# Kernel optimization log

Measured on AMD Instinct MI355X. Metric: run time of the kernel, lower is better.

Reference implementation:

```python
import jax, jax.numpy as jnp
import numpy as np

# Fixed problem sizes (uniform frames so the irregular loop vectorizes)
S = 32            # number of frames (sequences)
N = 128           # pedestrians per frame
H = 64            # pool_h_dim (lstm hidden dim)
G = 8             # grid_size
NS = 2.0          # neighbourhood_size
OUT = 64          # pool_out_dim
EPS = 1e-5        # BatchNorm1d eps


def setup_inputs() -> dict:
    key = jax.random.key(0)
    k1, k2, k3 = jax.random.split(key, 3)
    hidden_states = jax.random.normal(k1, (S * N, H), jnp.float32)
    # positions in [0, 4): neighbourhood of size 2 captures many neighbours
    all_pos = jax.random.uniform(k2, (S * N, 2), jnp.float32) * 4.0
    W = jax.random.normal(k3, (G * G * H, OUT), jnp.float32) * 0.02
    b = jnp.zeros((OUT,), jnp.float32)
    gamma = jnp.ones((OUT,), jnp.float32)
    beta = jnp.zeros((OUT,), jnp.float32)
    starts = jnp.arange(S, dtype=jnp.int32) * N
    seq_start_end = jnp.stack([starts, starts + N], axis=1)
    return {"hidden_states": hidden_states, "all_pos": all_pos, "W": W,
            "b": b, "gamma": gamma, "beta": beta,
            "seq_start_end": seq_start_end}


def _pool_one_frame(hs, ps):
    # hs: [N, H] hidden states, ps: [N, 2] positions of one frame.
    # Pair (i, j): bbox around ped i, contribution from ped j's hidden state.
    xi, yi = ps[:, 0][:, None], ps[:, 1][:, None]   # bbox owner i -> rows
    xj, yj = ps[:, 0][None, :], ps[:, 1][None, :]   # neighbour j -> cols
    half = NS / 2
    tlx, tly = xi - half, yi + half                 # top-left of bbox(i)
    brx, bry = xi + half, yi - half                 # bottom-right of bbox(i)
    gx = jnp.floor((xj - tlx) / NS * G)
    gy = jnp.floor((tly - yj) / NS * G)
    grid = (gx + G * gy).astype(jnp.int32) + 1      # +1: slot 0 is dump bin
    # out-of-bbox or self -> masked to bin 0
    mask = ((xj <= tlx) | (yj >= tly) | (xj >= brx) | (yj <= bry)
            | jnp.eye(N, dtype=bool))
    grid = grid + (jnp.arange(N, dtype=jnp.int32) * (G * G))[:, None]
    grid = jnp.where(mask, 0, grid)                 # [N, N]
    vals = jnp.broadcast_to(hs[None, :, :], (N, N, H)).reshape(N * N, H)
    pooled = jax.ops.segment_sum(vals, grid.reshape(-1),
                                 num_segments=N * G * G + 1)[1:]
    return pooled.reshape(N, G * G * H)


def reference(hidden_states, all_pos, W, b, gamma, beta, seq_start_end):
    h = hidden_states.reshape(S, N, H)
    p = all_pos.reshape(S, N, 2)
    pool_h = jax.vmap(_pool_one_frame)(h, p).reshape(S * N, G * G * H)
    x = pool_h @ W + b
    # BatchNorm1d in training mode: biased batch statistics
    mean = jnp.mean(x, axis=0)
    var = jnp.mean((x - mean) ** 2, axis=0)
    x = (x - mean) / jnp.sqrt(var + EPS) * gamma + beta
    return jax.nn.relu(x)
```

## Files before the change

### kernel.cpp

```cpp
#include <hip/hip_runtime.h>
#include <math.h>

#define NFRAMES 32
#define NPED    128
#define HDIM    64
#define KDIM    4096
#define OUTD    64
#define EPSV    1e-5f
#define NBLK    256
#define MROW    16
#define PROW    4104
#define HROWW   68

typedef __attribute__((ext_vector_type(8))) short  short8;
typedef __attribute__((ext_vector_type(4))) float  floatx4;

static __device__ __forceinline__ unsigned short f2bf(float f) {
    union { float f; unsigned u; } v; v.f = f;
    unsigned r = v.u + 0x7fffu + ((v.u >> 16) & 1u);
    return (unsigned short)(r >> 16);
}
static __device__ __forceinline__ unsigned pk2bf(float a, float b) {
    return (unsigned)f2bf(a) | ((unsigned)f2bf(b) << 16);
}

static __device__ __forceinline__ int kperm(int k) {
    return (k & 0xC0F) | ((k >> 2) & 0x0F0) | ((k & 0x030) << 4);
}

__global__ void k_wt(const float* __restrict__ W, unsigned short* __restrict__ Wt) {
    __shared__ float T[64 * 65];
    const int t  = threadIdx.x;
    const int k0 = blockIdx.x * 64;
    #pragma unroll
    for (int it = 0; it < 8; ++it) {
        int idx = it * 512 + t;
        int kl = idx >> 6, o = idx & 63;
        T[kl * 65 + o] = W[(size_t)(k0 + kl) * OUTD + o];
    }
    __syncthreads();
    {
        int o  = t & 63;
        int kl = (t >> 6) * 8;
        unsigned pk[4];
        #pragma unroll
        for (int e = 0; e < 4; ++e)
            pk[e] = pk2bf(T[(kl + 2 * e) * 65 + o], T[(kl + 2 * e + 1) * 65 + o]);
        int klog = kperm(k0 + kl);
        int wn   = o >> 4;
        int q    = klog >> 10;
        int s    = (klog >> 5) & 31;
        int quad = (klog >> 3) & 3;
        int ln   = quad * 16 + (o & 15);
        unsigned short* dst = Wt + ((size_t)((wn * 4 + q) * 32 + s) * 64 + ln) * 8;
        *(uint4*)dst = (uint4){pk[0], pk[1], pk[2], pk[3]};
    }
}

__global__ __launch_bounds__(1024, 1) void k_fused(
    const float* __restrict__ hs, const float* __restrict__ pos,
    const unsigned short* __restrict__ Wt,
    float* __restrict__ x, float* __restrict__ psumT, float* __restrict__ psumsqT)
{
    __shared__ char SM[MROW * PROW * 2 + 2048];
    unsigned short* P    = (unsigned short*)SM;
    unsigned int*   HsTw = (unsigned int*)SM;
    float*          red  = (float*)SM;
    unsigned char*  CT   = (unsigned char*)(SM + MROW * PROW * 2);

    const int tid   = threadIdx.x;
    const int bid   = blockIdx.x;
    const int f     = bid >> 3;
    const int chunk = bid & 7;
    const int lane  = tid & 63;
    const int w     = tid >> 6;
    const int m     = lane & 15;
    const int quad  = lane >> 4;

    const float4* h4 = (const float4*)(hs + f * (NPED * HDIM));
    {
        int jp   = (tid & 31) + ((tid >> 9) << 5);
        int hidx = (tid >> 5) & 15;
        float4 va = h4[(2 * jp) * 16 + hidx];
        float4 vb = h4[(2 * jp + 1) * 16 + hidx];
        HsTw[(hidx * 4 + 0) * HROWW + jp] = pk2bf(va.x, vb.x);
        HsTw[(hidx * 4 + 1) * HROWW + jp] = pk2bf(va.y, vb.y);
        HsTw[(hidx * 4 + 2) * HROWW + jp] = pk2bf(va.z, vb.z);
        HsTw[(hidx * 4 + 3) * HROWW + jp] = pk2bf(va.w, vb.w);
    }
    const float2* pf = (const float2*)pos + f * NPED;
    const int i0 = chunk * 16;
    #pragma unroll
    for (int it = 0; it < 2; ++it) {
        int idx = it * 1024 + tid;
        int i = idx >> 7, j = idx & 127;
        float2 pi = pf[i0 + i];
        float2 pj = pf[j];
        float tlx = pi.x - 1.0f, tly = pi.y + 1.0f;
        bool valid = (pj.x > tlx) & (pj.y < tly) & (pj.x < pi.x + 1.0f) &
                     (pj.y > pi.y - 1.0f) & (j != i0 + i);
        int gx = (int)floorf((pj.x - tlx) * 4.0f);
        int gy = (int)floorf((tly - pj.y) * 4.0f);
        int c  = gx + 8 * gy;
        CT[i * NPED + j] = (valid && (unsigned)c < 64u) ? (unsigned char)c : 255;
    }
    __syncthreads();

    short8 Af[4][4];
    #pragma unroll
    for (int ht = 0; ht < 4; ++ht)
        #pragma unroll
        for (int kt = 0; kt < 4; ++kt)
            Af[ht][kt] = *(const short8*)&HsTw[(ht * 16 + m) * HROWW + kt * 16 + quad * 4];
    __syncthreads();

    {
        const int i = w;
        const unsigned char* ctRow = CT + i * NPED;
        #pragma unroll
        for (int ch = 0; ch < 2; ++ch) {
            floatx4 pa[4][2];
            #pragma unroll
            for (int ht = 0; ht < 4; ++ht)
                #pragma unroll
                for (int c2 = 0; c2 < 2; ++c2) pa[ht][c2] = (floatx4){0.f, 0.f, 0.f, 0.f};
            #pragma unroll
            for (int kt = 0; kt < 4; ++kt) {
                unsigned long long cb = *(const unsigned long long*)(ctRow + kt * 32 + quad * 8);
                unsigned lo = (unsigned)cb, hi = (unsigned)(cb >> 32);
                int b0 = (int)(lo & 255u), b1 = (int)((lo >> 8) & 255u);
                int b2 = (int)((lo >> 16) & 255u), b3 = (int)(lo >> 24);
                int b4 = (int)(hi & 255u), b5 = (int)((hi >> 8) & 255u);
                int b6 = (int)((hi >> 16) & 255u), b7 = (int)(hi >> 24);
                #pragma unroll
                for (int c2 = 0; c2 < 2; ++c2) {
                    const int tgt = (ch * 2 + c2) * 16 + m;
                    union { int iv[4]; short8 sv; } B;
                    B.iv[0] = (b0 == tgt ? 0x00003F80 : 0) | (b1 == tgt ? 0x3F800000 : 0);
                    B.iv[1] = (b2 == tgt ? 0x00003F80 : 0) | (b3 == tgt ? 0x3F800000 : 0);
                    B.iv[2] = (b4 == tgt ? 0x00003F80 : 0) | (b5 == tgt ? 0x3F800000 : 0);
                    B.iv[3] = (b6 == tgt ? 0x00003F80 : 0) | (b7 == tgt ? 0x3F800000 : 0);
                    #pragma unroll
                    for (int ht = 0; ht < 4; ++ht)
                        pa[ht][c2] = __builtin_amdgcn_mfma_f32_16x16x32_bf16(Af[ht][kt], B.sv, pa[ht][c2], 0, 0, 0);
                }
            }
            #pragma unroll
            for (int c2 = 0; c2 < 2; ++c2)
                #pragma unroll
                for (int ht = 0; ht < 4; ++ht) {
                    union { floatx4 fv; unsigned uv[4]; } U; U.fv = pa[ht][c2];
                    uint2 pv;
                    pv.x = __builtin_amdgcn_perm(U.uv[1], U.uv[0], 0x07060302u);
                    pv.y = __builtin_amdgcn_perm(U.uv[3], U.uv[2], 0x07060302u);
                    *reinterpret_cast<uint2*>(&P[i * PROW + (ch * 2 + c2) * 1024 + ht * 256 + m * 16 + quad * 4]) = pv;
                }
        }
    }
    __syncthreads();

    const int wn = w & 3;
    const int wq = w >> 2;
    floatx4 acc[4];
    #pragma unroll
    for (int u = 0; u < 4; ++u) acc[u] = (floatx4){0.f, 0.f, 0.f, 0.f};
    const unsigned short* Prow = P + m * PROW + wq * 1024;
    const unsigned short* wB   = Wt + ((size_t)(wn * 4 + wq) * 32 * 64 + lane) * 8;
    #pragma unroll 8
    for (int s = 0; s < 32; ++s) {
        short8 a = *(const short8*)(Prow + s * 32 + quad * 8);
        short8 b = *(const short8*)(wB + s * 512);
        acc[s & 3] = __builtin_amdgcn_mfma_f32_16x16x32_bf16(a, b, acc[s & 3], 0, 0, 0);
    }
    floatx4 accf = (acc[0] + acc[1]) + (acc[2] + acc[3]);
    __syncthreads();

    if (wq != 0) *(floatx4*)(red + (((wq - 1) * 4 + wn) * 64 + lane) * 4) = accf;
    __syncthreads();

    if (wq == 0) {
        accf += *(const floatx4*)(red + ((0 * 4 + wn) * 64 + lane) * 4);
        accf += *(const floatx4*)(red + ((1 * 4 + wn) * 64 + lane) * 4);
        accf += *(const floatx4*)(red + ((2 * 4 + wn) * 64 + lane) * 4);
        const int ibase = f * NPED + chunk * 16;
        float s1 = 0.f, s2 = 0.f;
        #pragma unroll
        for (int r = 0; r < 4; ++r) {
            float v = accf[r];
            int row = quad * 4 + r;
            x[(size_t)(ibase + row) * OUTD + wn * 16 + m] = v;
            s1 += v; s2 += v * v;
        }
        s1 += __shfl_xor(s1, 16); s1 += __shfl_xor(s1, 32);
        s2 += __shfl_xor(s2, 16); s2 += __shfl_xor(s2, 32);
        if (lane < 16) {
            psumT  [(wn * 16 + lane) * NBLK + bid] = s1;
            psumsqT[(wn * 16 + lane) * NBLK + bid] = s2;
        }
    }
}

__global__ __launch_bounds__(512) void k_apply(
    const float* __restrict__ x, const float* __restrict__ psumT,
    const float* __restrict__ psumsqT, const float* __restrict__ gamma,
    const float* __restrict__ beta, float* __restrict__ out) {
    __shared__ float muL[OUTD], isL[OUTD];
    const int t = threadIdx.x;
    const int o = t >> 3, p = t & 7;
    float s1 = 0.f, s2 = 0.f;
    const float4* q1 = (const float4*)(psumT   + o * NBLK + p * 32);
    const float4* q2 = (const float4*)(psumsqT + o * NBLK + p * 32);
    #pragma unroll
    for (int i = 0; i < 8; ++i) {
        float4 a = q1[i], b = q2[i];
        s1 += (a.x + a.y) + (a.z + a.w);
        s2 += (b.x + b.y) + (b.z + b.w);
    }
    #pragma unroll
    for (int d = 1; d < 8; d <<= 1) {
        s1 += __shfl_xor(s1, d);
        s2 += __shfl_xor(s2, d);
    }
    if (p == 0) {
        const float inv_n = 1.0f / (float)(NFRAMES * NPED);
        float mu  = s1 * inv_n;
        float var = s2 * inv_n - mu * mu;
        muL[o] = mu;
        isL[o] = rsqrtf(var + EPSV);
    }
    __syncthreads();
    #pragma unroll
    for (int i = 0; i < 4; ++i) {
        int g  = blockIdx.x * 2048 + i * 512 + t;
        int o0 = (g & 15) * 4;
        float4 xv = ((const float4*)x)[g];
        float4 r;
        r.x = (xv.x - muL[o0 + 0]) * isL[o0 + 0] * gamma[o0 + 0] + beta[o0 + 0];
        r.y = (xv.y - muL[o0 + 1]) * isL[o0 + 1] * gamma[o0 + 1] + beta[o0 + 1];
        r.z = (xv.z - muL[o0 + 2]) * isL[o0 + 2] * gamma[o0 + 2] + beta[o0 + 2];
        r.w = (xv.w - muL[o0 + 3]) * isL[o0 + 3] * gamma[o0 + 3] + beta[o0 + 3];
        r.x = r.x > 0.f ? r.x : 0.f;
        r.y = r.y > 0.f ? r.y : 0.f;
        r.z = r.z > 0.f ? r.z : 0.f;
        r.w = r.w > 0.f ? r.w : 0.f;
        ((float4*)out)[g] = r;
    }
}

extern "C" void kernel_launch(void* const* d_in, const int* in_sizes, int n_in,
                              void* d_out, int out_size, void* d_ws, size_t ws_size,
                              hipStream_t stream) {
    const float* hs    = (const float*)d_in[0];
    const float* pos   = (const float*)d_in[1];
    const float* W     = (const float*)d_in[2];
    const float* gamma = (const float*)d_in[4];
    const float* beta  = (const float*)d_in[5];

    char* ws = (char*)d_ws;
    unsigned short* Wt = (unsigned short*)ws;
    float* x       = (float*)(ws + (512 << 10));
    float* psumT   = (float*)(ws + (512 << 10) + (1 << 20));
    float* psumsqT = psumT + NBLK * OUTD;

    k_wt   <<<KDIM / 64, 512, 0, stream>>>(W, Wt);
    k_fused<<<NBLK, 1024, 0, stream>>>(hs, pos, Wt, x, psumT, psumsqT);
    k_apply<<<32, 512, 0, stream>>>(x, psumT, psumsqT, gamma, beta, (float*)d_out);
}
```

Before: 87.05 us.

## Merge weight transpose, pooling GEMM and batchnorm into one cooperative kernel

Replaces the three launches (weight transpose/convert, fused pool+GEMM, batchnorm apply) with a single cooperative kernel. Each block converts a 16-row slice of W to bf16 in the permuted layout, then a grid-wide sync separates that from the GEMM. A second grid sync follows the per-block partial sums, after which every block reduces the batch statistics itself and applies normalization and ReLU directly from its accumulators. This removes two launch gaps and the round trip of the intermediate x through global memory. In exchange it adds two grid barriers and redundant statistics reduction in all 256 blocks, and it requires all 256 blocks of 1024 threads to be co-resident.

```diff
diff --git a/kernel.cpp b/kernel.cpp
--- a/kernel.cpp
+++ b/kernel.cpp
@@ -1,5 +1,8 @@
 #include <hip/hip_runtime.h>
+#include <hip/hip_cooperative_groups.h>
 #include <math.h>
+
+namespace cg = cooperative_groups;
 
 #define NFRAMES 32
 #define NPED    128
@@ -28,44 +31,20 @@
     return (k & 0xC0F) | ((k >> 2) & 0x0F0) | ((k & 0x030) << 4);
 }
 
-__global__ void k_wt(const float* __restrict__ W, unsigned short* __restrict__ Wt) {
-    __shared__ float T[64 * 65];
-    const int t  = threadIdx.x;
-    const int k0 = blockIdx.x * 64;
-    #pragma unroll
-    for (int it = 0; it < 8; ++it) {
-        int idx = it * 512 + t;
-        int kl = idx >> 6, o = idx & 63;
-        T[kl * 65 + o] = W[(size_t)(k0 + kl) * OUTD + o];
-    }
-    __syncthreads();
-    {
-        int o  = t & 63;
-        int kl = (t >> 6) * 8;
-        unsigned pk[4];
-        #pragma unroll
-        for (int e = 0; e < 4; ++e)
-            pk[e] = pk2bf(T[(kl + 2 * e) * 65 + o], T[(kl + 2 * e + 1) * 65 + o]);
-        int klog = kperm(k0 + kl);
-        int wn   = o >> 4;
-        int q    = klog >> 10;
-        int s    = (klog >> 5) & 31;
-        int quad = (klog >> 3) & 3;
-        int ln   = quad * 16 + (o & 15);
-        unsigned short* dst = Wt + ((size_t)((wn * 4 + q) * 32 + s) * 64 + ln) * 8;
-        *(uint4*)dst = (uint4){pk[0], pk[1], pk[2], pk[3]};
-    }
-}
-
-__global__ __launch_bounds__(1024, 1) void k_fused(
+__global__ __launch_bounds__(1024, 1) void k_all(
     const float* __restrict__ hs, const float* __restrict__ pos,
-    const unsigned short* __restrict__ Wt,
-    float* __restrict__ x, float* __restrict__ psumT, float* __restrict__ psumsqT)
+    const float* __restrict__ W, const float* __restrict__ gamma,
+    const float* __restrict__ beta, unsigned short* __restrict__ Wt,
+    float* __restrict__ psumT, float* __restrict__ psumsqT,
+    float* __restrict__ out)
 {
     __shared__ char SM[MROW * PROW * 2 + 2048];
     unsigned short* P    = (unsigned short*)SM;
     unsigned int*   HsTw = (unsigned int*)SM;
     float*          red  = (float*)SM;
+    float*          muL  = (float*)(SM + 16384);
+    float*          isL  = (float*)(SM + 16640);
+    float*          Tw   = (float*)(SM + 24576);
     unsigned char*  CT   = (unsigned char*)(SM + MROW * PROW * 2);
 
     const int tid   = threadIdx.x;
@@ -76,7 +55,13 @@
     const int w     = tid >> 6;
     const int m     = lane & 15;
     const int quad  = lane >> 4;
-
+    const int wn    = w & 3;
+    const int wq    = w >> 2;
+
+    {
+        int kl = tid >> 6, o = tid & 63;
+        Tw[kl * 65 + o] = W[(size_t)(bid * 16 + kl) * OUTD + o];
+    }
     const float4* h4 = (const float4*)(hs + f * (NPED * HDIM));
     {
         int jp   = (tid & 31) + ((tid >> 9) << 5);
@@ -106,6 +91,22 @@
     }
     __syncthreads();
 
+    if (tid < 128) {
+        int o  = tid & 63;
+        int kl = (tid >> 6) * 8;
+        unsigned pk[4];
+        #pragma unroll
+        for (int e = 0; e < 4; ++e)
+            pk[e] = pk2bf(Tw[(kl + 2 * e) * 65 + o], Tw[(kl + 2 * e + 1) * 65 + o]);
+        int klog = kperm(bid * 16 + kl);
+        int on   = o >> 4;
+        int q    = klog >> 10;
+        int s    = (klog >> 5) & 31;
+        int qd   = (klog >> 3) & 3;
+        int ln   = qd * 16 + (o & 15);
+        unsigned short* dst = Wt + ((size_t)((on * 4 + q) * 32 + s) * 64 + ln) * 8;
+        *(uint4*)dst = (uint4){pk[0], pk[1], pk[2], pk[3]};
+    }
     short8 Af[4][4];
     #pragma unroll
     for (int ht = 0; ht < 4; ++ht)
@@ -115,8 +116,7 @@
     __syncthreads();
 
     {
-        const int i = w;
-        const unsigned char* ctRow = CT + i * NPED;
+        const unsigned char* ctRow = CT + w * NPED;
         #pragma unroll
         for (int ch = 0; ch < 2; ++ch) {
             floatx4 pa[4][2];
@@ -153,14 +153,14 @@
                     uint2 pv;
                     pv.x = __builtin_amdgcn_perm(U.uv[1], U.uv[0], 0x07060302u);
                     pv.y = __builtin_amdgcn_perm(U.uv[3], U.uv[2], 0x07060302u);
-                    *reinterpret_cast<uint2*>(&P[i * PROW + (ch * 2 + c2) * 1024 + ht * 256 + m * 16 + quad * 4]) = pv;
+                    *reinterpret_cast<uint2*>(&P[w * PROW + (ch * 2 + c2) * 1024 + ht * 256 + m * 16 + quad * 4]) = pv;
                 }
         }
     }
     __syncthreads();
 
-    const int wn = w & 3;
-    const int wq = w >> 2;
+    cg::this_grid().sync();
+
     floatx4 acc[4];
     #pragma unroll
     for (int u = 0; u < 4; ++u) acc[u] = (floatx4){0.f, 0.f, 0.f, 0.f};
@@ -182,15 +182,9 @@
         accf += *(const floatx4*)(red + ((0 * 4 + wn) * 64 + lane) * 4);
         accf += *(const floatx4*)(red + ((1 * 4 + wn) * 64 + lane) * 4);
         accf += *(const floatx4*)(red + ((2 * 4 + wn) * 64 + lane) * 4);
-        const int ibase = f * NPED + chunk * 16;
         float s1 = 0.f, s2 = 0.f;
         #pragma unroll
-        for (int r = 0; r < 4; ++r) {
-            float v = accf[r];
-            int row = quad * 4 + r;
-            x[(size_t)(ibase + row) * OUTD + wn * 16 + m] = v;
-            s1 += v; s2 += v * v;
-        }
+        for (int r = 0; r < 4; ++r) { s1 += accf[r]; s2 += accf[r] * accf[r]; }
         s1 += __shfl_xor(s1, 16); s1 += __shfl_xor(s1, 32);
         s2 += __shfl_xor(s2, 16); s2 += __shfl_xor(s2, 32);
         if (lane < 16) {
@@ -198,52 +192,47 @@
             psumsqT[(wn * 16 + lane) * NBLK + bid] = s2;
         }
     }
-}
-
-__global__ __launch_bounds__(512) void k_apply(
-    const float* __restrict__ x, const float* __restrict__ psumT,
-    const float* __restrict__ psumsqT, const float* __restrict__ gamma,
-    const float* __restrict__ beta, float* __restrict__ out) {
-    __shared__ float muL[OUTD], isL[OUTD];
-    const int t = threadIdx.x;
-    const int o = t >> 3, p = t & 7;
-    float s1 = 0.f, s2 = 0.f;
-    const float4* q1 = (const float4*)(psumT   + o * NBLK + p * 32);
-    const float4* q2 = (const float4*)(psumsqT + o * NBLK + p * 32);
-    #pragma unroll
-    for (int i = 0; i < 8; ++i) {
-        float4 a = q1[i], b = q2[i];
-        s1 += (a.x + a.y) + (a.z + a.w);
-        s2 += (b.x + b.y) + (b.z + b.w);
-    }
-    #pragma unroll
-    for (int d = 1; d < 8; d <<= 1) {
-        s1 += __shfl_xor(s1, d);
-        s2 += __shfl_xor(s2, d);
-    }
-    if (p == 0) {
-        const float inv_n = 1.0f / (float)(NFRAMES * NPED);
-        float mu  = s1 * inv_n;
-        float var = s2 * inv_n - mu * mu;
-        muL[o] = mu;
-        isL[o] = rsqrtf(var + EPSV);
-    }
-    __syncthreads();
-    #pragma unroll
-    for (int i = 0; i < 4; ++i) {
-        int g  = blockIdx.x * 2048 + i * 512 + t;
-        int o0 = (g & 15) * 4;
-        float4 xv = ((const float4*)x)[g];
-        float4 r;
-        r.x = (xv.x - muL[o0 + 0]) * isL[o0 + 0] * gamma[o0 + 0] + beta[o0 + 0];
-        r.y = (xv.y - muL[o0 + 1]) * isL[o0 + 1] * gamma[o0 + 1] + beta[o0 + 1];
-        r.z = (xv.z - muL[o0 + 2]) * isL[o0 + 2] * gamma[o0 + 2] + beta[o0 + 2];
-        r.w = (xv.w - muL[o0 + 3]) * isL[o0 + 3] * gamma[o0 + 3] + beta[o0 + 3];
-        r.x = r.x > 0.f ? r.x : 0.f;
-        r.y = r.y > 0.f ? r.y : 0.f;
-        r.z = r.z > 0.f ? r.z : 0.f;
-        r.w = r.w > 0.f ? r.w : 0.f;
-        ((float4*)out)[g] = r;
+
+    cg::this_grid().sync();
+
+    {
+        int o = tid >> 4, p = tid & 15;
+        float s1 = 0.f, s2 = 0.f;
+        const float4* q1 = (const float4*)(psumT   + o * NBLK + p * 16);
+        const float4* q2 = (const float4*)(psumsqT + o * NBLK + p * 16);
+        #pragma unroll
+        for (int i = 0; i < 4; ++i) {
+            float4 a = q1[i], b = q2[i];
+            s1 += (a.x + a.y) + (a.z + a.w);
+            s2 += (b.x + b.y) + (b.z + b.w);
+        }
+        #pragma unroll
+        for (int d = 1; d < 16; d <<= 1) {
+            s1 += __shfl_xor(s1, d);
+            s2 += __shfl_xor(s2, d);
+        }
+        if (p == 0) {
+            const float inv_n = 1.0f / (float)(NFRAMES * NPED);
+            float mu  = s1 * inv_n;
+            float var = s2 * inv_n - mu * mu;
+            muL[o] = mu;
+            isL[o] = rsqrtf(var + EPSV);
+        }
+    }
+    __syncthreads();
+
+    if (wq == 0) {
+        const int o  = wn * 16 + m;
+        const float mu = muL[o], is = isL[o];
+        const float ga = gamma[o], be = beta[o];
+        const int ibase = f * NPED + chunk * 16;
+        #pragma unroll
+        for (int r = 0; r < 4; ++r) {
+            float v = (accf[r] - mu) * is * ga + be;
+            v = v > 0.f ? v : 0.f;
+            int row = quad * 4 + r;
+            out[(size_t)(ibase + row) * OUTD + o] = v;
+        }
     }
 }
 
@@ -258,11 +247,12 @@
 
     char* ws = (char*)d_ws;
     unsigned short* Wt = (unsigned short*)ws;
-    float* x       = (float*)(ws + (512 << 10));
-    float* psumT   = (float*)(ws + (512 << 10) + (1 << 20));
+    float* psumT   = (float*)(ws + (512 << 10));
     float* psumsqT = psumT + NBLK * OUTD;
-
-    k_wt   <<<KDIM / 64, 512, 0, stream>>>(W, Wt);
-    k_fused<<<NBLK, 1024, 0, stream>>>(hs, pos, Wt, x, psumT, psumsqT);
-    k_apply<<<32, 512, 0, stream>>>(x, psumT, psumsqT, gamma, beta, (float*)d_out);
-}
+    float* outp    = (float*)d_out;
+
+    void* args[] = {(void*)&hs, (void*)&pos, (void*)&W, (void*)&gamma, (void*)&beta,
+                    (void*)&Wt, (void*)&psumT, (void*)&psumsqT, (void*)&outp};
+    hipLaunchCooperativeKernel((const void*)k_all, dim3(NBLK), dim3(1024),
+                               args, 0, stream);
+}
```

Measured after the change: 149.9 us. +72.2%, slower.
